# Performance work log

Hardware: AMD Instinct MI355X
Metric: run time of the kernel (lower is better)

## Reference

```python
import jax, jax.numpy as jnp
import numpy as np

N_COUNTRIES = 8
ADJ = jnp.array([
    [0, 1, 1, 1, 1, 1, 1, 0],
    [1, 0, 1, 0, 0, 0, 0, 1],
    [1, 1, 0, 1, 0, 1, 0, 0],
    [1, 0, 1, 0, 1, 1, 1, 0],
    [1, 0, 0, 1, 0, 1, 1, 0],
    [1, 0, 1, 1, 1, 0, 0, 0],
    [1, 0, 0, 1, 1, 0, 0, 0],
    [0, 1, 0, 0, 0, 0, 0, 0]], dtype=jnp.float32)
GDP = jnp.array([0.4, 0.15, 0.12, 0.1, 0.08, 0.08, 0.05, 0.02], dtype=jnp.float32)

B, D_IN, H, NH, L = 8192, 512, 256, 4, 3
HD = H * NH  # 1024: QKV width (no head reshape in the original)


def layer_norm(x, g, b, eps=1e-5):
    m = x.mean(-1, keepdims=True)
    v = ((x - m) ** 2).mean(-1, keepdims=True)
    return (x - m) * jax.lax.rsqrt(v + eps) * g + b


def setup_inputs() -> dict:
    key = jax.random.key(0)
    ks = jax.random.split(key, 12)
    lin = lambda k, i, o: (jax.random.normal(k, (i, o), jnp.float32) / np.sqrt(i).astype(np.float32))
    lin3 = lambda k, i, o: (jax.random.normal(k, (L, i, o), jnp.float32) / np.sqrt(i).astype(np.float32))
    return {
        'regional_features': jax.random.normal(ks[0], (B, D_IN), jnp.float32),
        'Wi': lin(ks[1], D_IN, H), 'bi': jnp.zeros((H,), jnp.float32),
        'emb': 0.02 * jax.random.normal(ks[2], (N_COUNTRIES, H), jnp.float32),
        'Wq': lin3(ks[3], H, HD), 'bq': jnp.zeros((L, HD), jnp.float32),
        'Wk': lin3(ks[4], H, HD), 'bk': jnp.zeros((L, HD), jnp.float32),
        'Wv': lin3(ks[5], H, HD), 'bv': jnp.zeros((L, HD), jnp.float32),
        'Wo': lin3(ks[6], HD, H), 'bo': jnp.zeros((L, H), jnp.float32),
        'ln_g': jnp.ones((L, H), jnp.float32), 'ln_b': jnp.zeros((L, H), jnp.float32),
        'Wp': lin(ks[7], H, H), 'bp': jnp.zeros((H,), jnp.float32),
        'lnp_g': jnp.ones((H,), jnp.float32), 'lnp_b': jnp.zeros((H,), jnp.float32),
    }


def reference(regional_features, Wi, bi, emb, Wq, bq, Wk, bk, Wv, bv, Wo, bo,
              ln_g, ln_b, Wp, bp, lnp_g, lnp_b):
    # input projection + broadcast over the 8 countries + country embedding
    h = regional_features @ Wi + bi                     # [B, H]
    x = h[:, None, :] + emb[None, :, :]                 # [B, 8, H]
    scale = 1.0 / np.sqrt(H).astype(np.float32)         # sqrt(dim)=sqrt(256), as in original
    mask = ADJ == 0                                     # [8, 8]
    for l in range(L):
        Q = x @ Wq[l] + bq[l]                           # [B, 8, HD]
        K = x @ Wk[l] + bk[l]
        V = x @ Wv[l] + bv[l]
        scores = jnp.einsum('bnd,bmd->bnm', Q, K) * scale  # [B, 8, 8]
        scores = jnp.where(mask[None], -jnp.inf, scores)
        attn = jax.nn.softmax(scores, axis=-1)          # dropout is identity in eval
        out = jnp.einsum('bnm,bmd->bnd', attn, V)       # [B, 8, HD]
        out = out @ Wo[l] + bo[l]                       # [B, 8, H]
        x = layer_norm(x + out, ln_g[l], ln_b[l])
    regional = jnp.sum(x * GDP[None, :, None], axis=1)  # [B, H]
    p = layer_norm(regional @ Wp + bp, lnp_g, lnp_b)
    return jax.nn.gelu(p, approximate=False)            # torch nn.GELU default = exact erf
```

## Files before the change

kernel.cpp:

```cpp
#include <hip/hip_runtime.h>
#include <hip/hip_bf16.h>
#include <math.h>


typedef short bf16x8 __attribute__((ext_vector_type(8)));
typedef float f32x4  __attribute__((ext_vector_type(4)));

__device__ __forceinline__ float bflo(unsigned int u){ return __uint_as_float(u << 16); }
__device__ __forceinline__ float bfhi(unsigned int u){ return __uint_as_float(u & 0xffff0000u); }
__device__ __forceinline__ float bfs(short s){ return __uint_as_float((unsigned int)(unsigned short)s << 16); }
__device__ __forceinline__ unsigned short f2bf(float f){
  __hip_bfloat16 h = __float2bfloat16(f);
  return *reinterpret_cast<unsigned short*>(&h);
}
__device__ __forceinline__ int gsw(int r, int q){ return (r + 16*q) ^ (r >> 2); }
__device__ __forceinline__ void unpack8(uint4 a, float* o){
  o[0]=bflo(a.x); o[1]=bfhi(a.x); o[2]=bflo(a.y); o[3]=bfhi(a.y);
  o[4]=bflo(a.z); o[5]=bfhi(a.z); o[6]=bflo(a.w); o[7]=bfhi(a.w);
}
__device__ __forceinline__ uint4 pack8(const float* v){
  uint4 r;
  r.x = (unsigned int)f2bf(v[0]) | ((unsigned int)f2bf(v[1]) << 16);
  r.y = (unsigned int)f2bf(v[2]) | ((unsigned int)f2bf(v[3]) << 16);
  r.z = (unsigned int)f2bf(v[4]) | ((unsigned int)f2bf(v[5]) << 16);
  r.w = (unsigned int)f2bf(v[6]) | ((unsigned int)f2bf(v[7]) << 16);
  return r;
}
__device__ __forceinline__ void gload16(const void* g, void* l){
  __builtin_amdgcn_global_load_lds(
      (const __attribute__((address_space(1))) unsigned int*)g,
      (__attribute__((address_space(3))) unsigned int*)l, 16, 0, 0);
}
__device__ __forceinline__ bf16x8 shfl8(bf16x8 v, int src){
  union U { bf16x8 h; int u[4]; };
  U a, r; a.h = v;
  #pragma unroll
  for (int j = 0; j < 4; j++) r.u[j] = __shfl(a.u[j], src);
  return r.h;
}
__device__ __forceinline__ bf16x8 pk8(const float* v){
  bf16x8 r;
  #pragma unroll
  for (int j = 0; j < 8; j++) r[j] = (short)f2bf(v[j]);
  return r;
}
__device__ __forceinline__ int pidx(int n, int k){
  return (k >> 5)*8192 + (n >> 4)*512 + ((k >> 3) & 3)*128 + (n & 15)*8 + (k & 7);
}

struct P1P {
  const float* csrc[3]; short* cdst[3];
  const float* tsrc[5]; short* tdst[5];
  int trows[5]; int tcols[5]; int tpack[5]; int toff[6];
};
__global__ __launch_bounds__(256) void k_prep1(P1P p){
  __shared__ float tile[64][65];
  int bid = blockIdx.x;
  if (bid < 1152){
    int s = bid / 384, lb = bid % 384;
    size_t e = (size_t)lb * 2048 + (size_t)threadIdx.x * 8;
    const float* src = p.csrc[s] + e;
    float4 v0 = *(const float4*)src;
    float4 v1 = *(const float4*)(src + 4);
    float v[8] = {v0.x,v0.y,v0.z,v0.w,v1.x,v1.y,v1.z,v1.w};
    *(uint4*)(p.cdst[s] + e) = pack8(v);
    return;
  }
  int tb = bid - 1152, s = 0;
  while (tb >= p.toff[s+1]) s++;
  int ti = tb - p.toff[s];
  int cols = p.tcols[s], rows = p.trows[s];
  int ntc = cols >> 6;
  int r0 = (ti / ntc) * 64, c0 = (ti % ntc) * 64;
  const float* src = p.tsrc[s];
  int row = threadIdx.x >> 2, jb = (threadIdx.x & 3) * 16;
  #pragma unroll
  for (int j = 0; j < 16; j += 4){
    float4 v = *(const float4*)(src + (size_t)(r0 + row) * cols + c0 + jb + j);
    tile[row][jb+j] = v.x; tile[row][jb+j+1] = v.y; tile[row][jb+j+2] = v.z; tile[row][jb+j+3] = v.w;
  }
  __syncthreads();
  short* dst = p.tdst[s];
  float tmp[16];
  #pragma unroll
  for (int j = 0; j < 16; j++) tmp[j] = tile[jb + j][row];
  if (p.tpack[s]){
    int n = c0 + row;
    #pragma unroll
    for (int gq = 0; gq < 2; gq++){
      int k = r0 + jb + gq*8;
      *(uint4*)(dst + pidx(n, k)) = pack8(&tmp[gq*8]);
    }
  } else {
    #pragma unroll
    for (int j = 0; j < 16; j += 8)
      *(uint4*)(dst + (size_t)(c0 + row) * rows + r0 + jb + j) = pack8(&tmp[j]);
  }
}

struct GD2 { const short* A; const short* Bt; short* Cp; float scale; };
struct P2P {
  GD2 d[6];
  const short* Wkb; const short* WoTb;
  const float* bq; const float* bv; const float* bo;
  float* ck; float* cvo;
};
__global__ __launch_bounds__(256) void k_prep2(P2P p){
  __shared__ alignas(16) short As[64*128];
  __shared__ alignas(16) short Bs[64*128];
  __shared__ float sv[1024];
  const int bid = blockIdx.x, tid = threadIdx.x;
  if (bid < 96){
    const int lane = tid & 63, w = tid >> 6;
    const int wm = w >> 1, wn = w & 1;
    const int z = bid >> 4, rem = bid & 15, bx = rem >> 2, by = rem & 3;
    GD2 g = p.d[z];
    const int K = 1024;
    f32x4 acc[2][2] = {};
    for (int k0 = 0; k0 < K; k0 += 128){
      #pragma unroll
      for (int kc = 0; kc < 4; kc++){
        int ro = w*16 + (lane & 15);
        int co = k0 + kc*32 + (lane >> 4)*8;
        gload16(g.A  + (size_t)(bx*64 + ro)*K + co, &As[(kc*4 + w)*512]);
        gload16(g.Bt + (size_t)(by*64 + ro)*K + co, &Bs[(kc*4 + w)*512]);
      }
      __syncthreads();
      #pragma unroll
      for (int kc = 0; kc < 4; kc++){
        bf16x8 av[2], bv[2];
        #pragma unroll
        for (int mi = 0; mi < 2; mi++)
          av[mi] = *(const bf16x8*)&As[((kc*4 + wm*2 + mi)*64 + lane)*8];
        #pragma unroll
        for (int nj = 0; nj < 2; nj++)
          bv[nj] = *(const bf16x8*)&Bs[((kc*4 + wn*2 + nj)*64 + lane)*8];
        #pragma unroll
        for (int mi = 0; mi < 2; mi++)
          #pragma unroll
          for (int nj = 0; nj < 2; nj++)
            acc[mi][nj] = __builtin_amdgcn_mfma_f32_16x16x32_bf16(av[mi], bv[nj], acc[mi][nj], 0, 0, 0);
      }
      __syncthreads();
    }
    #pragma unroll
    for (int mi = 0; mi < 2; mi++)
      #pragma unroll
      for (int nj = 0; nj < 2; nj++)
        #pragma unroll
        for (int j = 0; j < 4; j++){
          int r = bx*64 + wm*32 + mi*16 + (lane >> 4)*4 + j;
          int c = by*64 + wn*32 + nj*16 + (lane & 15);
          g.Cp[pidx(r, c)] = (short)f2bf(acc[mi][nj][j] * g.scale);
        }
    return;
  }
  int v = bid - 96;
  int job = v / 3, l = v % 3;
  const short* rows = (job == 0 ? p.Wkb : p.WoTb) + (size_t)l*262144;
  const float* vec  = (job == 0 ? p.bq : p.bv) + l*1024;
  const float scale = (job == 0) ? 0.0625f : 1.0f;
  for (int i = tid; i < 1024; i += 256) sv[i] = vec[i];
  __syncthreads();
  const int row = tid >> 3, sub = tid & 7;
  for (int pass = 0; pass < 8; pass++){
    int r = pass*32 + row;
    const short* rp = rows + (size_t)r*1024;
    float acc = 0.f;
    #pragma unroll
    for (int i = 0; i < 16; i++){
      int d = sub*8 + i*64;
      uint4 vv = *(const uint4*)(rp + d);
      float f[8]; unpack8(vv, f);
      #pragma unroll
      for (int j = 0; j < 8; j++) acc = fmaf(f[j], sv[d + j], acc);
    }
    acc += __shfl_xor(acc, 1); acc += __shfl_xor(acc, 2); acc += __shfl_xor(acc, 4);
    if (sub == 0){
      float o = acc * scale;
      if (job == 1) o += p.bo[l*256 + r];
      (job == 0 ? p.ck : p.cvo)[l*256 + r] = o;
    }
  }
}

__global__ __launch_bounds__(512, 2) void k_net(
    const float* __restrict__ rf, const short* __restrict__ WiT,
    const float* __restrict__ bi, const float* __restrict__ emb,
    const short* __restrict__ Wqk, const short* __restrict__ Wvo,
    const float* __restrict__ ckv, const float* __restrict__ cvov,
    const float* __restrict__ lng, const float* __restrict__ lnb,
    const short* __restrict__ WpT, const float* __restrict__ bpv,
    const float* __restrict__ lpg, const float* __restrict__ lpb,
    float* __restrict__ outp){
  const int tid = threadIdx.x, lane = tid & 63, w = tid >> 6;
  const int b0 = blockIdx.x * 16;
  const int dsub = (lane >> 4) * 8;
  const int glane = gsw(lane & 15, lane >> 4);
  __shared__ alignas(16) short tst[8][4096];
  __shared__ alignas(16) short wbuf[32768];
  __shared__ alignas(16) float atn[8][16][16];
  __shared__ short ckb[256];
  __shared__ float s_add[256], s_g[256], s_b[256];
  __shared__ float redS[8][16], redQ[8][16], s_mean[16], s_rstd[16];

  #define LKW  asm volatile("s_waitcnt lgkmcnt(0)" ::: "memory")
  #define VMW0 asm volatile("s_waitcnt vmcnt(0)" ::: "memory")

  auto STAGEW = [&](const short* W, int h){
    #pragma unroll
    for (int i = 0; i < 8; i++)
      gload16(W + (size_t)(w*16 + h*8 + i)*512 + lane*8, &wbuf[(w*8 + i)*512]);
  };

  float* hst  = (float*)&tst[0][0];
  float* embs = hst + 16*264;
  float* bis  = embs + 2048;
  if (tid < 256) bis[tid] = bi[tid];
  for (int i = tid; i < 2048; i += 512) embs[i] = emb[i];
  f32x4 hacc[2] = {};
  #pragma unroll
  for (int kk = 0; kk < 16; kk++){
    const float* ap = rf + (size_t)(b0 + (lane & 15)) * 512 + kk*32 + dsub;
    float4 a0 = *(const float4*)ap, a1 = *(const float4*)(ap + 4);
    float af[8] = {a0.x,a0.y,a0.z,a0.w,a1.x,a1.y,a1.z,a1.w};
    bf16x8 av = pk8(af);
    #pragma unroll
    for (int nj = 0; nj < 2; nj++){
      bf16x8 bv = *(const bf16x8*)(WiT + (size_t)(kk*16 + w*2 + nj)*512 + lane*8);
      hacc[nj] = __builtin_amdgcn_mfma_f32_16x16x32_bf16(av, bv, hacc[nj], 0, 0, 0);
    }
  }
  __syncthreads();
  #pragma unroll
  for (int nj = 0; nj < 2; nj++)
    #pragma unroll
    for (int jj = 0; jj < 4; jj++){
      int m = (lane >> 4)*4 + jj, col = w*32 + nj*16 + (lane & 15);
      hst[m*264 + col] = hacc[nj][jj] + bis[col];
    }
  __syncthreads();
  bf16x8 xf[8];
  {
    int r15 = lane & 15;
    int bt = w*2 + (r15 >> 3), ct = r15 & 7;
    #pragma unroll
    for (int c = 0; c < 8; c++){
      float v8[8];
      #pragma unroll
      for (int e = 0; e < 8; e++){
        int d = dsub + 32*c + e;
        v8[e] = hst[bt*264 + d] + embs[ct*256 + d];
      }
      xf[c] = pk8(v8);
    }
  }

  const unsigned long long MASK64 = 0x02191D69752B857EULL;

  #pragma unroll 1
  for (int l = 0; l < 3; ++l){
    __syncthreads();
    if (tid < 256){
      ckb[tid]   = (short)f2bf(ckv[l*256 + tid]);
      s_add[tid] = cvov[l*256 + tid];
      s_g[tid]   = lng[l*256 + tid];
      s_b[tid]   = lnb[l*256 + tid];
    }
    const short* Wq_ = Wqk + l*65536;
    const short* Wv_ = Wvo + l*65536;
    STAGEW(Wq_, 0);
    VMW0; __syncthreads();

    f32x4 sacc = {0.f, 0.f, 0.f, 0.f};
    #pragma unroll
    for (int h = 0; h < 2; h++){
      f32x4 acc[8] = {};
      #pragma unroll
      for (int kk = 0; kk < 8; kk++)
        #pragma unroll
        for (int nj = 0; nj < 8; nj++){
          bf16x8 bv = *(const bf16x8*)&wbuf[(kk*8 + nj)*512 + lane*8];
          acc[nj] = __builtin_amdgcn_mfma_f32_16x16x32_bf16(xf[kk], bv, acc[nj], 0, 0, 0);
        }
      if (h == 0){ __syncthreads(); STAGEW(Wq_, 1); }
      #pragma unroll
      for (int nj = 0; nj < 8; nj++)
        #pragma unroll
        for (int jj = 0; jj < 4; jj++){
          int i_ = (lane >> 4)*4 + jj, nl = nj*16 + (lane & 15);
          tst[w][(nl >> 5)*512 + gsw(i_, (nl >> 3) & 3)*8 + (nl & 7)] = (short)f2bf(acc[nj][jj]);
        }
      LKW; __builtin_amdgcn_sched_barrier(0);
      #pragma unroll
      for (int cl = 0; cl < 4; cl++){
        bf16x8 tf = *(const bf16x8*)&tst[w][cl*512 + glane*8];
        sacc = __builtin_amdgcn_mfma_f32_16x16x32_bf16(tf, xf[h*4 + cl], sacc, 0, 0, 0);
      }
      LKW;
      if (h == 0){ VMW0; __syncthreads(); }
    }
    __syncthreads();
    STAGEW(Wv_, 0);

    float skv = 0.f;
    #pragma unroll
    for (int c = 0; c < 8; c++){
      bf16x8 cv = *(const bf16x8*)&ckb[c*32 + dsub];
      #pragma unroll
      for (int e = 0; e < 8; e++) skv = fmaf(bfs(xf[c][e]), bfs(cv[e]), skv);
    }
    skv += __shfl_xor(skv, 16); skv += __shfl_xor(skv, 32);

    #pragma unroll
    for (int jj = 0; jj < 4; jj++){
      int i_ = (lane >> 4)*4 + jj, j_ = lane & 15;
      bool ok = (((i_ ^ j_) & 8) == 0) &&
                ((MASK64 >> (((i_ & 7) << 3) | (j_ & 7))) & 1ull);
      float sv = ok ? (sacc[jj] + skv) : -3.0e38f;
      float mx = sv;
      mx = fmaxf(mx, __shfl_xor(mx, 1));
      mx = fmaxf(mx, __shfl_xor(mx, 2));
      mx = fmaxf(mx, __shfl_xor(mx, 4));
      float e = ok ? __expf(sv - mx) : 0.f;
      float sum = e;
      sum += __shfl_xor(sum, 1); sum += __shfl_xor(sum, 2); sum += __shfl_xor(sum, 4);
      atn[w][i_][j_] = e / sum;
    }
    LKW;

    bf16x8 yfrag[8];
    {
      float4 A0 = *(const float4*)&atn[w][lane & 15][lane & 8];
      float4 A1 = *(const float4*)&atn[w][lane & 15][(lane & 8) + 4];
      float am[8] = {A0.x, A0.y, A0.z, A0.w, A1.x, A1.y, A1.z, A1.w};
      #pragma unroll
      for (int c = 0; c < 8; c++){
        float a8[8] = {0,0,0,0,0,0,0,0};
        #pragma unroll
        for (int mi = 0; mi < 8; mi++){
          bf16x8 xs = shfl8(xf[c], (lane & 48) | (lane & 8) | mi);
          #pragma unroll
          for (int e = 0; e < 8; e++) a8[e] = fmaf(am[mi], bfs(xs[e]), a8[e]);
        }
        yfrag[c] = pk8(a8);
      }
    }
    VMW0; __syncthreads();

    float rs = 0.f, rq = 0.f;
    float* fst = (float*)&tst[w][0];
    #pragma unroll
    for (int h = 0; h < 2; h++){
      f32x4 acc[8] = {};
      #pragma unroll
      for (int kk = 0; kk < 8; kk++)
        #pragma unroll
        for (int nj = 0; nj < 8; nj++){
          bf16x8 bv = *(const bf16x8*)&wbuf[(kk*8 + nj)*512 + lane*8];
          acc[nj] = __builtin_amdgcn_mfma_f32_16x16x32_bf16(yfrag[kk], bv, acc[nj], 0, 0, 0);
        }
      if (h == 0){ __syncthreads(); STAGEW(Wv_, 1); }
      #pragma unroll
      for (int nj = 0; nj < 8; nj++)
        #pragma unroll
        for (int jj = 0; jj < 4; jj++){
          int i_ = (lane >> 4)*4 + jj;
          int dq = nj*16 + (lane & 15);
          fst[(dq >> 5)*512 + gsw(i_, (dq >> 3) & 3)*8 + (dq & 7)] = acc[nj][jj];
        }
      LKW; __builtin_amdgcn_sched_barrier(0);
      #pragma unroll
      for (int lc = 0; lc < 4; lc++){
        int c = h*4 + lc;
        float v8[8];
        #pragma unroll
        for (int e = 0; e < 8; e++){
          int d = 32*c + dsub + e;
          float t = fst[lc*512 + glane*8 + e] + s_add[d] + bfs(xf[c][e]);
          rs += t; rq = fmaf(t, t, rq);
          v8[e] = t;
        }
        xf[c] = pk8(v8);
      }
      LKW;
      if (h == 0){ VMW0; __syncthreads(); }
    }
    rs += __shfl_xor(rs, 16); rs += __shfl_xor(rs, 32);
    rq += __shfl_xor(rq, 16); rq += __shfl_xor(rq, 32);
    float mn = rs * (1.f/256.f);
    float var = rq * (1.f/256.f) - mn*mn;
    float rr = rsqrtf(fmaxf(var, 0.f) + 1e-5f);
    #pragma unroll
    for (int c = 0; c < 8; c++){
      float v8[8];
      #pragma unroll
      for (int e = 0; e < 8; e++){
        int d = 32*c + dsub + e;
        v8[e] = (bfs(xf[c][e]) - mn) * rr * s_g[d] + s_b[d];
      }
      xf[c] = pk8(v8);
    }
  }

  __syncthreads();
  short* Ast = &tst[0][0];
  {
    int c7 = lane & 7;
    float g = (c7 == 0) ? 0.4f : (c7 == 1) ? 0.15f : (c7 == 2) ? 0.12f :
              (c7 == 3) ? 0.1f : (c7 == 4) ? 0.08f : (c7 == 5) ? 0.08f :
              (c7 == 6) ? 0.05f : 0.02f;
    #pragma unroll
    for (int c = 0; c < 8; c++){
      float v8[8];
      #pragma unroll
      for (int e = 0; e < 8; e++){
        float v = g * bfs(xf[c][e]);
        v += __shfl_xor(v, 1); v += __shfl_xor(v, 2); v += __shfl_xor(v, 4);
        v8[e] = v;
      }
      if ((lane & 7) == 0){
        int bt = w*2 + ((lane >> 3) & 1);
        *(bf16x8*)&Ast[bt*264 + dsub + 32*c] = pk8(v8);
      }
    }
  }
  __syncthreads();
  f32x4 ha[2] = {};
  #pragma unroll
  for (int kk = 0; kk < 8; kk++){
    bf16x8 av = *(const bf16x8*)&Ast[(lane & 15)*264 + kk*32 + dsub];
    #pragma unroll
    for (int nj = 0; nj < 2; nj++){
      bf16x8 bv = *(const bf16x8*)(WpT + (size_t)(kk*16 + w*2 + nj)*512 + lane*8);
      ha[nj] = __builtin_amdgcn_mfma_f32_16x16x32_bf16(av, bv, ha[nj], 0, 0, 0);
    }
  }
  #pragma unroll
  for (int jj = 0; jj < 4; jj++){
    float s = 0.f, q = 0.f;
    #pragma unroll
    for (int nj = 0; nj < 2; nj++){
      int cx = w*32 + nj*16 + (lane & 15);
      float t = ha[nj][jj] + bpv[cx];
      ha[nj][jj] = t;
      s += t; q = fmaf(t, t, q);
    }
    s += __shfl_xor(s, 1); q += __shfl_xor(q, 1);
    s += __shfl_xor(s, 2); q += __shfl_xor(q, 2);
    s += __shfl_xor(s, 4); q += __shfl_xor(q, 4);
    s += __shfl_xor(s, 8); q += __shfl_xor(q, 8);
    if ((lane & 15) == 0){
      int rl = (lane >> 4)*4 + jj;
      redS[w][rl] = s; redQ[w][rl] = q;
    }
  }
  __syncthreads();
  if (tid < 16){
    float sm = 0.f, sq = 0.f;
    #pragma unroll
    for (int w2 = 0; w2 < 8; w2++){ sm += redS[w2][tid]; sq += redQ[w2][tid]; }
    float mn = sm * (1.f/256.f);
    float var = sq * (1.f/256.f) - mn*mn;
    s_mean[tid] = mn;
    s_rstd[tid] = rsqrtf(fmaxf(var, 0.f) + 1e-5f);
  }
  __syncthreads();
  #pragma unroll
  for (int jj = 0; jj < 4; jj++){
    int rl = (lane >> 4)*4 + jj;
    float mn = s_mean[rl], rstd = s_rstd[rl];
    #pragma unroll
    for (int nj = 0; nj < 2; nj++){
      int cx = w*32 + nj*16 + (lane & 15);
      float y = (ha[nj][jj] - mn) * rstd * lpg[cx] + lpb[cx];
      outp[(size_t)(b0 + rl)*256 + cx] = 0.5f * y * (1.0f + erff(y * 0.70710678118654752f));
    }
  }
  #undef LKW
  #undef VMW0
}

extern "C" void kernel_launch(void* const* d_in, const int* in_sizes, int n_in,
                              void* d_out, int out_size, void* d_ws, size_t ws_size,
                              hipStream_t stream){
  (void)in_sizes; (void)n_in; (void)out_size; (void)ws_size;
  const float* rf  = (const float*)d_in[0];
  const float* Wi  = (const float*)d_in[1];
  const float* bi  = (const float*)d_in[2];
  const float* emb = (const float*)d_in[3];
  const float* Wq  = (const float*)d_in[4];
  const float* bq  = (const float*)d_in[5];
  const float* Wk  = (const float*)d_in[6];
  const float* bk  = (const float*)d_in[7];
  const float* Wv  = (const float*)d_in[8];
  const float* bv  = (const float*)d_in[9];
  const float* Wo  = (const float*)d_in[10];
  const float* bo  = (const float*)d_in[11];
  const float* lng = (const float*)d_in[12];
  const float* lnb = (const float*)d_in[13];
  const float* Wp  = (const float*)d_in[14];
  const float* bp  = (const float*)d_in[15];
  const float* lpg = (const float*)d_in[16];
  const float* lpb = (const float*)d_in[17];
  (void)bk;

  char* ws = (char*)d_ws;
  short* Wqb  = (short*)(ws);
  short* Wkb  = (short*)(ws + 1572864ull);
  short* Wvb  = (short*)(ws + 3145728ull);
  short* WoTb = (short*)(ws + 4718592ull);
  short* WqkP = (short*)(ws + 6291456ull);
  short* WvoP = (short*)(ws + 6684672ull);
  short* WiTP = (short*)(ws + 7077888ull);
  short* WpTP = (short*)(ws + 7340032ull);
  float* ckv  = (float*)(ws + 7471104ull);
  float* cvov = (float*)(ws + 7474176ull);

  { P1P p;
    p.csrc[0]=Wq; p.cdst[0]=Wqb;
    p.csrc[1]=Wk; p.cdst[1]=Wkb;
    p.csrc[2]=Wv; p.cdst[2]=Wvb;
    p.tsrc[0]=Wi;        p.tdst[0]=WiTP;          p.trows[0]=512;  p.tcols[0]=256; p.tpack[0]=1;
    p.tsrc[1]=Wo;        p.tdst[1]=WoTb;          p.trows[1]=1024; p.tcols[1]=256; p.tpack[1]=0;
    p.tsrc[2]=Wo+262144; p.tdst[2]=WoTb+262144;   p.trows[2]=1024; p.tcols[2]=256; p.tpack[2]=0;
    p.tsrc[3]=Wo+524288; p.tdst[3]=WoTb+524288;   p.trows[3]=1024; p.tcols[3]=256; p.tpack[3]=0;
    p.tsrc[4]=Wp;        p.tdst[4]=WpTP;          p.trows[4]=256;  p.tcols[4]=256; p.tpack[4]=1;
    p.toff[0]=0; p.toff[1]=32; p.toff[2]=96; p.toff[3]=160; p.toff[4]=224; p.toff[5]=240;
    k_prep1<<<dim3(1392), dim3(256), 0, stream>>>(p); }

  { P2P p;
    for (int l = 0; l < 3; l++){
      p.d[l]   = GD2{ Wkb  + l*262144, Wqb + l*262144, WqkP + l*65536, 0.0625f };
      p.d[3+l] = GD2{ WoTb + l*262144, Wvb + l*262144, WvoP + l*65536, 1.0f };
    }
    p.Wkb = Wkb; p.WoTb = WoTb;
    p.bq = bq; p.bv = bv; p.bo = bo;
    p.ck = ckv; p.cvo = cvov;
    k_prep2<<<dim3(102), dim3(256), 0, stream>>>(p); }

  k_net<<<dim3(512), dim3(512), 0, stream>>>(rf, WiTP, bi, emb, WqkP, WvoP,
      ckv, cvov, lng, lnb, WpTP, bp, lpg, lpb, (float*)d_out);
}
```

Measured before the change: 206.4 us.

## Stream layer weights through a 4-slot LDS ring buffer with per-chunk prefetch

Replaces the half-matrix weight staging (64KB LDS buffer with full syncthreads and vmcnt(0) waits) with a 4-slot ring of 8KB chunks. Each chunk is prefetched three steps ahead across all layers and both matmul phases, and waits are relaxed to vmcnt(2) plus a bare barrier. LDS use shrinks further by preloading all three layers' per-layer constants once (gamma/beta stored as bf16), storing the Wo output tile as bf16, and reusing the atn buffer for reductions. The smaller LDS footprint may allow more blocks per CU. The cost is a barrier per K-chunk and lower precision in the residual and LayerNorm inputs.

```diff
diff --git a/kernel.cpp b/kernel.cpp
--- a/kernel.cpp
+++ b/kernel.cpp
@@ -197,20 +197,25 @@
   const int b0 = blockIdx.x * 16;
   const int dsub = (lane >> 4) * 8;
   const int glane = gsw(lane & 15, lane >> 4);
-  __shared__ alignas(16) short tst[8][4096];
-  __shared__ alignas(16) short wbuf[32768];
+  __shared__ alignas(16) short tst[8][2048];
+  __shared__ alignas(16) short wbuf[4][4096];
   __shared__ alignas(16) float atn[8][16][16];
-  __shared__ short ckb[256];
-  __shared__ float s_add[256], s_g[256], s_b[256];
-  __shared__ float redS[8][16], redQ[8][16], s_mean[16], s_rstd[16];
+  __shared__ short ckb3[768];
+  __shared__ float sadd3[768];
+  __shared__ short sg3[768];
+  __shared__ short sb3[768];
 
   #define LKW  asm volatile("s_waitcnt lgkmcnt(0)" ::: "memory")
   #define VMW0 asm volatile("s_waitcnt vmcnt(0)" ::: "memory")
-
-  auto STAGEW = [&](const short* W, int h){
-    #pragma unroll
-    for (int i = 0; i < 8; i++)
-      gload16(W + (size_t)(w*16 + h*8 + i)*512 + lane*8, &wbuf[(w*8 + i)*512]);
+  #define VMW1 asm volatile("s_waitcnt vmcnt(1)" ::: "memory")
+  #define VMW2 asm volatile("s_waitcnt vmcnt(2)" ::: "memory")
+  #define BAR  __builtin_amdgcn_s_barrier()
+
+  auto STAGE = [&](int n){
+    int cc = n & 15;
+    const short* W = (((n >> 4) & 1) ? Wvo : Wqk) + (n >> 5)*65536;
+    const short* src = W + ((((cc & 7)*16 + (cc >> 3)*8) << 9) + tid*8);
+    gload16(src, &wbuf[n & 3][tid*8]);
   };
 
   float* hst  = (float*)&tst[0][0];
@@ -231,6 +236,12 @@
       hacc[nj] = __builtin_amdgcn_mfma_f32_16x16x32_bf16(av, bv, hacc[nj], 0, 0, 0);
     }
   }
+  for (int i = tid; i < 768; i += 512){
+    ckb3[i]  = (short)f2bf(ckv[i]);
+    sadd3[i] = cvov[i];
+    sg3[i]   = (short)f2bf(lng[i]);
+    sb3[i]   = (short)f2bf(lnb[i]);
+  }
   __syncthreads();
   #pragma unroll
   for (int nj = 0; nj < 2; nj++)
@@ -255,35 +266,35 @@
       xf[c] = pk8(v8);
     }
   }
+  VMW0; __syncthreads();
+  STAGE(0); STAGE(1); STAGE(2);
 
   const unsigned long long MASK64 = 0x02191D69752B857EULL;
 
   #pragma unroll 1
   for (int l = 0; l < 3; ++l){
-    __syncthreads();
-    if (tid < 256){
-      ckb[tid]   = (short)f2bf(ckv[l*256 + tid]);
-      s_add[tid] = cvov[l*256 + tid];
-      s_g[tid]   = lng[l*256 + tid];
-      s_b[tid]   = lnb[l*256 + tid];
-    }
-    const short* Wq_ = Wqk + l*65536;
-    const short* Wv_ = Wvo + l*65536;
-    STAGEW(Wq_, 0);
-    VMW0; __syncthreads();
+    const short* ckb  = ckb3  + l*256;
+    const float* sadd = sadd3 + l*256;
+    const short* sg   = sg3   + l*256;
+    const short* sb   = sb3   + l*256;
+    const bool lgl = (l == 2);
 
     f32x4 sacc = {0.f, 0.f, 0.f, 0.f};
     #pragma unroll
     for (int h = 0; h < 2; h++){
       f32x4 acc[8] = {};
       #pragma unroll
-      for (int kk = 0; kk < 8; kk++)
+      for (int kk = 0; kk < 8; kk++){
+        const int n = l*32 + h*8 + kk;
+        VMW2; BAR;
+        STAGE(n + 3);
+        const short* P = &wbuf[n & 3][0];
         #pragma unroll
         for (int nj = 0; nj < 8; nj++){
-          bf16x8 bv = *(const bf16x8*)&wbuf[(kk*8 + nj)*512 + lane*8];
+          bf16x8 bv = *(const bf16x8*)&P[nj*512 + lane*8];
           acc[nj] = __builtin_amdgcn_mfma_f32_16x16x32_bf16(xf[kk], bv, acc[nj], 0, 0, 0);
         }
-      if (h == 0){ __syncthreads(); STAGEW(Wq_, 1); }
+      }
       #pragma unroll
       for (int nj = 0; nj < 8; nj++)
         #pragma unroll
@@ -298,10 +309,7 @@
         sacc = __builtin_amdgcn_mfma_f32_16x16x32_bf16(tf, xf[h*4 + cl], sacc, 0, 0, 0);
       }
       LKW;
-      if (h == 0){ VMW0; __syncthreads(); }
-    }
-    __syncthreads();
-    STAGEW(Wv_, 0);
+    }
 
     float skv = 0.f;
     #pragma unroll
@@ -346,28 +354,32 @@
         yfrag[c] = pk8(a8);
       }
     }
-    VMW0; __syncthreads();
 
     float rs = 0.f, rq = 0.f;
-    float* fst = (float*)&tst[w][0];
     #pragma unroll
     for (int h = 0; h < 2; h++){
       f32x4 acc[8] = {};
       #pragma unroll
-      for (int kk = 0; kk < 8; kk++)
+      for (int kk = 0; kk < 8; kk++){
+        const int c = h*8 + kk;
+        const int n = l*32 + 16 + c;
+        if (lgl && c == 14){ VMW1; } else if (lgl && c == 15){ VMW0; } else { VMW2; }
+        BAR;
+        if (!(lgl && c >= 13)) STAGE(n + 3);
+        const short* P = &wbuf[n & 3][0];
         #pragma unroll
         for (int nj = 0; nj < 8; nj++){
-          bf16x8 bv = *(const bf16x8*)&wbuf[(kk*8 + nj)*512 + lane*8];
+          bf16x8 bv = *(const bf16x8*)&P[nj*512 + lane*8];
           acc[nj] = __builtin_amdgcn_mfma_f32_16x16x32_bf16(yfrag[kk], bv, acc[nj], 0, 0, 0);
         }
-      if (h == 0){ __syncthreads(); STAGEW(Wv_, 1); }
+      }
       #pragma unroll
       for (int nj = 0; nj < 8; nj++)
         #pragma unroll
         for (int jj = 0; jj < 4; jj++){
           int i_ = (lane >> 4)*4 + jj;
           int dq = nj*16 + (lane & 15);
-          fst[(dq >> 5)*512 + gsw(i_, (dq >> 3) & 3)*8 + (dq & 7)] = acc[nj][jj];
+          tst[w][(dq >> 5)*512 + gsw(i_, (dq >> 3) & 3)*8 + (dq & 7)] = (short)f2bf(acc[nj][jj]);
         }
       LKW; __builtin_amdgcn_sched_barrier(0);
       #pragma unroll
@@ -377,14 +389,13 @@
         #pragma unroll
         for (int e = 0; e < 8; e++){
           int d = 32*c + dsub + e;
-          float t = fst[lc*512 + glane*8 + e] + s_add[d] + bfs(xf[c][e]);
+          float t = bfs(tst[w][lc*512 + glane*8 + e]) + sadd[d] + bfs(xf[c][e]);
           rs += t; rq = fmaf(t, t, rq);
           v8[e] = t;
         }
         xf[c] = pk8(v8);
       }
       LKW;
-      if (h == 0){ VMW0; __syncthreads(); }
     }
     rs += __shfl_xor(rs, 16); rs += __shfl_xor(rs, 32);
     rq += __shfl_xor(rq, 16); rq += __shfl_xor(rq, 32);
@@ -397,7 +408,7 @@
       #pragma unroll
       for (int e = 0; e < 8; e++){
         int d = 32*c + dsub + e;
-        v8[e] = (bfs(xf[c][e]) - mn) * rr * s_g[d] + s_b[d];
+        v8[e] = (bfs(xf[c][e]) - mn) * rr * bfs(sg[d]) + bfs(sb[d]);
       }
       xf[c] = pk8(v8);
     }
@@ -426,6 +437,10 @@
     }
   }
   __syncthreads();
+  float* redS  = &atn[0][0][0];
+  float* redQ  = redS + 128;
+  float* s_mn  = redQ + 128;
+  float* s_rs  = s_mn + 16;
   f32x4 ha[2] = {};
   #pragma unroll
   for (int kk = 0; kk < 8; kk++){
@@ -452,24 +467,24 @@
     s += __shfl_xor(s, 8); q += __shfl_xor(q, 8);
     if ((lane & 15) == 0){
       int rl = (lane >> 4)*4 + jj;
-      redS[w][rl] = s; redQ[w][rl] = q;
+      redS[w*16 + rl] = s; redQ[w*16 + rl] = q;
     }
   }
   __syncthreads();
   if (tid < 16){
     float sm = 0.f, sq = 0.f;
     #pragma unroll
-    for (int w2 = 0; w2 < 8; w2++){ sm += redS[w2][tid]; sq += redQ[w2][tid]; }
+    for (int w2 = 0; w2 < 8; w2++){ sm += redS[w2*16 + tid]; sq += redQ[w2*16 + tid]; }
     float mn = sm * (1.f/256.f);
     float var = sq * (1.f/256.f) - mn*mn;
-    s_mean[tid] = mn;
-    s_rstd[tid] = rsqrtf(fmaxf(var, 0.f) + 1e-5f);
+    s_mn[tid] = mn;
+    s_rs[tid] = rsqrtf(fmaxf(var, 0.f) + 1e-5f);
   }
   __syncthreads();
   #pragma unroll
   for (int jj = 0; jj < 4; jj++){
     int rl = (lane >> 4)*4 + jj;
-    float mn = s_mean[rl], rstd = s_rstd[rl];
+    float mn = s_mn[rl], rstd = s_rs[rl];
     #pragma unroll
     for (int nj = 0; nj < 2; nj++){
       int cx = w*32 + nj*16 + (lane & 15);
@@ -479,6 +494,9 @@
   }
   #undef LKW
   #undef VMW0
+  #undef VMW1
+  #undef VMW2
+  #undef BAR
 }
 
 extern "C" void kernel_launch(void* const* d_in, const int* in_sizes, int n_in,
```

Result: slower. 213.6 us (+3.5%).
